# Performance work log

Hardware: AMD Instinct MI355X
Metric: run time of the kernel (lower is better)

Reference implementation:

```python
import jax, jax.numpy as jnp
import numpy as np

B, N, D, C = 1, 512, 128, 128
EPS = 1e-5


def _layernorm(x, g, b):
    m = jnp.mean(x, axis=-1, keepdims=True)
    v = jnp.mean(jnp.square(x - m), axis=-1, keepdims=True)
    return (x - m) * jax.lax.rsqrt(v + EPS) * g + b


def setup_inputs() -> dict:
    key = jax.random.key(0)
    ks = jax.random.split(key, 14)
    sD = 1.0 / np.sqrt(D)
    sC = 1.0 / np.sqrt(C)

    def w(k, shape, scale):
        return jax.random.normal(k, shape, dtype=jnp.float32) * scale

    return {
        "x": jax.random.normal(ks[0], (B, N, N, D), dtype=jnp.float32),
        "ln_in_g": jnp.ones((D,), jnp.float32),
        "ln_in_b": jnp.zeros((D,), jnp.float32),
        "ln_out_g": jnp.ones((C,), jnp.float32),
        "ln_out_b": jnp.zeros((C,), jnp.float32),
        "Wl": w(ks[1], (D, C), sD), "bl": w(ks[2], (C,), 0.02),
        "Wr": w(ks[3], (D, C), sD), "br": w(ks[4], (C,), 0.02),
        "Wo": w(ks[5], (C, D), sC), "bo": w(ks[6], (D,), 0.02),
        "Wlg": w(ks[7], (D, C), sD), "blg": w(ks[8], (C,), 0.02),
        "Wrg": w(ks[9], (D, C), sD), "brg": w(ks[10], (C,), 0.02),
        "Wog": w(ks[11], (D, D), sD), "bog": w(ks[12], (D,), 0.02),
    }


def reference(x, ln_in_g, ln_in_b, ln_out_g, ln_out_b,
              Wl, bl, Wr, br, Wo, bo, Wlg, blg, Wrg, brg, Wog, bog):
    # x: [B, N, N, D] pair representation
    xn = _layernorm(x, ln_in_g, ln_in_b)
    left = jax.nn.sigmoid(xn @ Wlg + blg) * (xn @ Wl + bl)    # [B,N,N,C]
    right = jax.nn.sigmoid(xn @ Wrg + brg) * (xn @ Wr + br)   # [B,N,N,C]
    # type='out': contract over k (rows): out[b,i,j,c] = sum_k left[b,k,i,c]*right[b,k,j,c]
    out = jnp.einsum('bkic,bkjc->bijc', left, right)           # [B,N,N,C]
    out = jax.nn.sigmoid(xn @ Wog + bog) * (_layernorm(out, ln_out_g, ln_out_b) @ Wo + bo)
    return out
```

## Files before the change

kernel.cpp:

```cpp
#include <hip/hip_runtime.h>
#include <hip/hip_bf16.h>
#include <cstdint>
#include <cstddef>

typedef unsigned short u16;
typedef short bf16x8 __attribute__((ext_vector_type(8)));
typedef float f32x4 __attribute__((ext_vector_type(4)));

constexpr int Ns = 512;
constexpr int Dd = 128;
constexpr int Cc = 128;
#define EPSV 1e-5f

__device__ __forceinline__ u16 f2bf(float f){
    __hip_bfloat16 h = __float2bfloat16(f);
    return *reinterpret_cast<u16*>(&h);
}
__device__ __forceinline__ float bf2f(u16 h){
    return __uint_as_float(((uint32_t)h) << 16);
}
__device__ __forceinline__ float sigmoidf_(float x){
    return 1.0f / (1.0f + __expf(-x));
}

__global__ void k_prep(const float* __restrict__ Wl, const float* __restrict__ Wlg,
                       const float* __restrict__ Wr, const float* __restrict__ Wrg,
                       const float* __restrict__ Wog, const float* __restrict__ Wo,
                       u16* __restrict__ Wt){
    int idx = blockIdx.x * 256 + threadIdx.x;
    if (idx >= 6 * 16384) return;
    int m = idx >> 14; int nk = idx & 16383; int n = nk >> 7; int k = nk & 127;
    const float* W = (m == 0) ? Wl : (m == 1) ? Wlg : (m == 2) ? Wr
                   : (m == 3) ? Wrg : (m == 4) ? Wog : Wo;
    Wt[idx] = f2bf(W[k * Cc + n]);
}

__global__ __launch_bounds__(256) void k1(
    const float* __restrict__ x, const float* __restrict__ g_ln, const float* __restrict__ b_ln,
    const u16* __restrict__ Wt,
    const float* __restrict__ bl, const float* __restrict__ blg,
    const float* __restrict__ br, const float* __restrict__ brg,
    const float* __restrict__ bog,
    u16* __restrict__ left, u16* __restrict__ right, u16* __restrict__ og)
{
    __shared__ u16  lA[64][136];
    __shared__ u16  lS[64][132];
    __shared__ float gln[128], bln[128];

    const int t   = threadIdx.x;
    const int bid = blockIdx.x;
    const int a0  = (bid >> 6) << 3;
    const int b0  = (bid & 63) << 3;
    const int w = t >> 6, l = t & 63;
    const int lrow = l & 15, g = l >> 4;
    const int nb = w * 32;
    const int orow = g << 2;
    const int kb = a0 >> 3;

    auto LOADP = [&](int mV, int mG, int cf, bf16x8 (&bv)[4], bf16x8 (&bg)[4]){
        const u16* WV = Wt + (size_t)mV * 16384;
        const u16* WG = Wt + (size_t)mG * 16384;
        const int col = nb + cf * 16 + lrow;
#pragma unroll
        for (int ks = 0; ks < 4; ++ks){
            bv[ks] = *reinterpret_cast<const bf16x8*>(WV + (size_t)col * 128 + ks * 32 + g * 8);
            bg[ks] = *reinterpret_cast<const bf16x8*>(WG + (size_t)col * 128 + ks * 32 + g * 8);
        }
    };
    auto LOAD1 = [&](int mV, int cf, bf16x8 (&bv)[4]){
        const u16* WV = Wt + (size_t)mV * 16384;
        const int col = nb + cf * 16 + lrow;
#pragma unroll
        for (int ks = 0; ks < 4; ++ks)
            bv[ks] = *reinterpret_cast<const bf16x8*>(WV + (size_t)col * 128 + ks * 32 + g * 8);
    };

    const int r = t >> 2, q = t & 3;
    const int aa = a0 + (r & 7), bb = b0 + (r >> 3);
    const float4* xrow = reinterpret_cast<const float4*>(x + ((size_t)aa * Ns + bb) * Dd);
    float4 xv[8];
#pragma unroll
    for (int i2 = 0; i2 < 8; ++i2) xv[i2] = xrow[q + 4 * i2];

    bf16x8 bvA[4], bgA[4], bvB[4], bgB[4];
    LOADP(0, 1, 0, bvA, bgA);

    if (t < 128){ gln[t] = g_ln[t]; bln[t] = b_ln[t]; }

    float s1 = 0.f, s2 = 0.f;
#pragma unroll
    for (int i2 = 0; i2 < 8; ++i2){
        float4 v = xv[i2];
        s1 += v.x + v.y + v.z + v.w;
        s2 += v.x * v.x + v.y * v.y + v.z * v.z + v.w * v.w;
    }
    s1 += __shfl_xor(s1, 1); s1 += __shfl_xor(s1, 2);
    s2 += __shfl_xor(s2, 1); s2 += __shfl_xor(s2, 2);
    const float mm  = s1 * (1.0f / 128.0f);
    const float rsv = rsqrtf(s2 * (1.0f / 128.0f) - mm * mm + EPSV);
    __syncthreads();
#pragma unroll
    for (int i2 = 0; i2 < 8; ++i2){
        const int d = (q + 4 * i2) * 4;
        ushort4 o;
        o.x = f2bf((xv[i2].x - mm) * rsv * gln[d + 0] + bln[d + 0]);
        o.y = f2bf((xv[i2].y - mm) * rsv * gln[d + 1] + bln[d + 1]);
        o.z = f2bf((xv[i2].z - mm) * rsv * gln[d + 2] + bln[d + 2]);
        o.w = f2bf((xv[i2].w - mm) * rsv * gln[d + 3] + bln[d + 3]);
        *reinterpret_cast<ushort4*>(&lA[r][d]) = o;
    }
    __syncthreads();

    bf16x8 af[4][4];
#pragma unroll
    for (int ks = 0; ks < 4; ++ks)
#pragma unroll
        for (int rf = 0; rf < 4; ++rf)
            af[ks][rf] = *reinterpret_cast<const bf16x8*>(&lA[rf * 16 + lrow][ks * 32 + g * 8]);

    const f32x4 zero4 = {0.f, 0.f, 0.f, 0.f};
    f32x4 aV[4], aG[4];
    auto Z2 = [&](){
#pragma unroll
        for (int rf = 0; rf < 4; ++rf){ aV[rf] = zero4; aG[rf] = zero4; }
    };
    auto MMVG = [&](const bf16x8 (&bv)[4], const bf16x8 (&bg)[4]){
#pragma unroll
        for (int ks = 0; ks < 4; ++ks){
#pragma unroll
            for (int rf = 0; rf < 4; ++rf)
                aV[rf] = __builtin_amdgcn_mfma_f32_16x16x32_bf16(af[ks][rf], bv[ks], aV[rf], 0, 0, 0);
#pragma unroll
            for (int rf = 0; rf < 4; ++rf)
                aG[rf] = __builtin_amdgcn_mfma_f32_16x16x32_bf16(af[ks][rf], bg[ks], aG[rf], 0, 0, 0);
        }
    };
    auto MMV = [&](const bf16x8 (&bv)[4]){
#pragma unroll
        for (int ks = 0; ks < 4; ++ks)
#pragma unroll
            for (int rf = 0; rf < 4; ++rf)
                aV[rf] = __builtin_amdgcn_mfma_f32_16x16x32_bf16(af[ks][rf], bv[ks], aV[rf], 0, 0, 0);
    };
    auto EPI1 = [&](u16* dst, const float* bV, const float* bG, int cf){
        const int col = nb + cf * 16 + lrow;
        const float bVv = bV[col], bGv = bG[col];
#pragma unroll
        for (int rf = 0; rf < 4; ++rf){
            ushort4 pk;
#pragma unroll
            for (int j = 0; j < 4; ++j){
                const float vv = aV[rf][j] + bVv;
                const float gg = aG[rf][j] + bGv;
                ((u16*)&pk)[j] = f2bf(sigmoidf_(gg) * vv);
            }
            const size_t base = (((size_t)col * 64 + kb) * Ns + b0 + rf * 2 + (orow >> 3)) * 8 + (orow & 4);
            *reinterpret_cast<ushort4*>(dst + base) = pk;
        }
    };
    auto OG1 = [&](int cf){
        const int col = nb + cf * 16 + lrow;
        const float bOv = bog[col];
#pragma unroll
        for (int rf = 0; rf < 4; ++rf)
#pragma unroll
            for (int j = 0; j < 4; ++j){
                const int row = rf * 16 + orow + j;
                lS[row][col] = f2bf(sigmoidf_(aV[rf][j] + bOv));
            }
    };

    LOADP(0, 1, 1, bvB, bgB);
    Z2(); MMVG(bvA, bgA); EPI1(left, bl, blg, 0);
    LOADP(2, 3, 0, bvA, bgA);
    Z2(); MMVG(bvB, bgB); EPI1(left, bl, blg, 1);
    LOADP(2, 3, 1, bvB, bgB);
    Z2(); MMVG(bvA, bgA); EPI1(right, br, brg, 0);
    LOAD1(4, 0, bvA);
    Z2(); MMVG(bvB, bgB); EPI1(right, br, brg, 1);
    LOAD1(4, 1, bvB);
#pragma unroll
    for (int rf = 0; rf < 4; ++rf) aV[rf] = zero4;
    MMV(bvA); OG1(0);
#pragma unroll
    for (int rf = 0; rf < 4; ++rf) aV[rf] = zero4;
    MMV(bvB); OG1(1);

    __syncthreads();
    const int bsub = t >> 5, c4 = (t & 31) * 4;
#pragma unroll
    for (int a = 0; a < 8; ++a){
        const int row = bsub * 8 + a;
        int2 v = *reinterpret_cast<const int2*>(&lS[row][c4]);
        *reinterpret_cast<int2*>(og + (((size_t)(a0 + a) * Ns) + (b0 + bsub)) * Cc + c4) = v;
    }
}

#define K2_LOAD(AF, BF, KS) do {                                                    \
    const size_t kbrow_ = (size_t)((KS) * 4 + lkb) * Ns;                            \
    _Pragma("unroll") for (int rf = 0; rf < 4; ++rf)                                \
        AF[rf] = *reinterpret_cast<const bf16x8*>(Lc + (kbrow_ + ib + rf * 16 + lrow) * 8); \
    _Pragma("unroll") for (int cf = 0; cf < 4; ++cf)                                \
        BF[cf] = *reinterpret_cast<const bf16x8*>(Rc + (kbrow_ + jb + cf * 16 + lrow) * 8); \
} while (0)

#define K2_MM(AF, BF) do {                                                          \
    _Pragma("unroll") for (int rf = 0; rf < 4; ++rf)                                \
    _Pragma("unroll") for (int cf = 0; cf < 4; ++cf)                                \
        acc[rf][cf] = __builtin_amdgcn_mfma_f32_16x16x32_bf16(AF[rf], BF[cf], acc[rf][cf], 0, 0, 0); \
} while (0)

__global__ __launch_bounds__(256) void k2(const u16* __restrict__ left,
                                          const u16* __restrict__ right,
                                          u16* __restrict__ om)
{
    __shared__ u16 sO[128][136];
    const int bid = blockIdx.x;
    const int xcd = bid & 7, idxx = bid >> 3;
    const int virt = xcd * 256 + idxx;
    const int c    = virt >> 4;
    const int tile = virt & 15;
    const int iy = tile >> 2, jx = tile & 3;
    const int t = threadIdx.x, w = t >> 6, l = t & 63;
    const int wr = w >> 1, wc = w & 1;
    const int ib = iy * 128 + wr * 64;
    const int jb = jx * 128 + wc * 64;
    const int lrow = l & 15, lkb = l >> 4;
    const u16* Lc = left  + (size_t)c * (Ns * Ns);
    const u16* Rc = right + (size_t)c * (Ns * Ns);
    const f32x4 zero4 = {0.f, 0.f, 0.f, 0.f};
    f32x4 acc[4][4];
#pragma unroll
    for (int rf = 0; rf < 4; ++rf)
#pragma unroll
        for (int cf = 0; cf < 4; ++cf) acc[rf][cf] = zero4;

    bf16x8 a0f[4], b0f[4], a1f[4], b1f[4];
    K2_LOAD(a0f, b0f, 0);
#pragma unroll
    for (int ks = 0; ks < 16; ks += 2){
        K2_LOAD(a1f, b1f, ks + 1);
        K2_MM(a0f, b0f);
        if (ks + 2 < 16) K2_LOAD(a0f, b0f, ks + 2);
        K2_MM(a1f, b1f);
    }

    const int orow = (l >> 4) << 2;
#pragma unroll
    for (int rf = 0; rf < 4; ++rf)
#pragma unroll
        for (int j2 = 0; j2 < 4; ++j2){
            const int rloc = wr * 64 + rf * 16 + orow + j2;
#pragma unroll
            for (int cf = 0; cf < 4; ++cf)
                sO[rloc][wc * 64 + cf * 16 + lrow] = f2bf(acc[rf][cf][j2]);
        }
    __syncthreads();
    u16* obase = om + (size_t)c * Ns * Ns + (size_t)(iy * 128) * Ns + jx * 128;
#pragma unroll
    for (int s = 0; s < 8; ++s){
        const int gg = s * 256 + t;
        const int row = gg >> 4, co = (gg & 15) * 8;
        int4 v = *reinterpret_cast<const int4*>(&sO[row][co]);
        *reinterpret_cast<int4*>(obase + (size_t)row * Ns + co) = v;
    }
}

__global__ __launch_bounds__(256) void k3(
    const u16* __restrict__ om, const u16* __restrict__ og, const u16* __restrict__ Wt,
    const float* __restrict__ g2, const float* __restrict__ b2, const float* __restrict__ bo,
    float* __restrict__ out)
{
    __shared__ char smem[34816];
    u16* X = reinterpret_cast<u16*>(smem);
    u16* O = reinterpret_cast<u16*>(smem) + 8704;
    __shared__ float sg2[128], sb2[128];
    const int i  = blockIdx.y;
    const int j0 = blockIdx.x * 64;
    const int t  = threadIdx.x;
    if (t < 128){ sg2[t] = g2[t]; sb2[t] = b2[t]; }
    {
        const int c = t >> 1, jh = (t & 1) * 32;
        const u16* src = om + (size_t)c * Ns * Ns + (size_t)i * Ns + j0 + jh;
#pragma unroll
        for (int s = 0; s < 8; ++s){
            ushort4 v = reinterpret_cast<const ushort4*>(src)[s];
            const int jj = jh + s * 4;
            X[(jj + 0) * 136 + c] = v.x; X[(jj + 1) * 136 + c] = v.y;
            X[(jj + 2) * 136 + c] = v.z; X[(jj + 3) * 136 + c] = v.w;
        }
    }
    {
        const int jj = t >> 2, qq = t & 3;
        const u16* src = og + ((size_t)i * Ns + j0 + jj) * Cc + qq * 32;
#pragma unroll
        for (int s = 0; s < 4; ++s)
            *reinterpret_cast<int4*>(&O[jj * 136 + qq * 32 + s * 8]) = reinterpret_cast<const int4*>(src)[s];
    }
    __syncthreads();
    const int r = t >> 2, q = t & 3;
    {
        float s1 = 0.f, s2v = 0.f;
#pragma unroll
        for (int e = 0; e < 32; ++e){
            const float v = bf2f(X[r * 136 + q * 32 + e]);
            s1 += v; s2v += v * v;
        }
        s1  += __shfl_xor(s1, 1);  s1  += __shfl_xor(s1, 2);
        s2v += __shfl_xor(s2v, 1); s2v += __shfl_xor(s2v, 2);
        const float mm  = s1 * (1.0f / 128.0f);
        const float rsv = rsqrtf(s2v * (1.0f / 128.0f) - mm * mm + EPSV);
#pragma unroll
        for (int e = 0; e < 32; ++e){
            const int cc = q * 32 + e;
            const float v = bf2f(X[r * 136 + cc]);
            X[r * 136 + cc] = f2bf((v - mm) * rsv * sg2[cc] + sb2[cc]);
        }
    }
    __syncthreads();
    const int w = t >> 6, l = t & 63;
    const int lrow = l & 15, lk = (l >> 4) << 3, nbv = w * 32, orow = (l >> 4) << 2;
    const u16* WO = Wt + (size_t)5 * 16384;
    const f32x4 zero4 = {0.f, 0.f, 0.f, 0.f};
    f32x4 acc[4][2];
#pragma unroll
    for (int rf = 0; rf < 4; ++rf)
#pragma unroll
        for (int cf = 0; cf < 2; ++cf) acc[rf][cf] = zero4;
#pragma unroll
    for (int ks = 0; ks < 4; ++ks){
        const int k0 = ks * 32 + lk;
        bf16x8 af[4];
#pragma unroll
        for (int rf = 0; rf < 4; ++rf)
            af[rf] = *reinterpret_cast<const bf16x8*>(&X[(rf * 16 + lrow) * 136 + k0]);
#pragma unroll
        for (int cf = 0; cf < 2; ++cf){
            bf16x8 bv = *reinterpret_cast<const bf16x8*>(WO + (size_t)(nbv + cf * 16 + lrow) * 128 + k0);
#pragma unroll
            for (int rf = 0; rf < 4; ++rf)
                acc[rf][cf] = __builtin_amdgcn_mfma_f32_16x16x32_bf16(af[rf], bv, acc[rf][cf], 0, 0, 0);
        }
    }
    float gv[2][4][4];
#pragma unroll
    for (int cf = 0; cf < 2; ++cf){
        const int cg = nbv + cf * 16 + lrow;
        const float bov = bo[cg];
#pragma unroll
        for (int rf = 0; rf < 4; ++rf)
#pragma unroll
            for (int j = 0; j < 4; ++j){
                const int row = rf * 16 + orow + j;
                gv[cf][rf][j] = bf2f(O[row * 136 + cg]) * (acc[rf][cf][j] + bov);
            }
    }
    __syncthreads();
    float* sF = reinterpret_cast<float*>(smem);
#pragma unroll
    for (int cf = 0; cf < 2; ++cf){
        const int cg = nbv + cf * 16 + lrow;
#pragma unroll
        for (int rf = 0; rf < 4; ++rf)
#pragma unroll
            for (int j = 0; j < 4; ++j){
                const int row = rf * 16 + orow + j;
                sF[row * 128 + cg] = gv[cf][rf][j];
            }
    }
    __syncthreads();
    const float4* sF4 = reinterpret_cast<const float4*>(smem);
    float* obase = out + ((size_t)i * Ns + j0) * Cc;
#pragma unroll
    for (int s = 0; s < 8; ++s){
        const int gg = s * 256 + t;
        const int row = gg >> 5, co = (gg & 31) * 4;
        float4 v = sF4[gg];
        *reinterpret_cast<float4*>(obase + (size_t)row * Cc + co) = v;
    }
}

extern "C" void kernel_launch(void* const* d_in, const int* in_sizes, int n_in,
                              void* d_out, int out_size, void* d_ws, size_t ws_size,
                              hipStream_t stream)
{
    const float* x    = (const float*)d_in[0];
    const float* ling = (const float*)d_in[1];
    const float* linb = (const float*)d_in[2];
    const float* loutg= (const float*)d_in[3];
    const float* loutb= (const float*)d_in[4];
    const float* Wl   = (const float*)d_in[5];
    const float* bl   = (const float*)d_in[6];
    const float* Wr   = (const float*)d_in[7];
    const float* br   = (const float*)d_in[8];
    const float* Wo   = (const float*)d_in[9];
    const float* bo   = (const float*)d_in[10];
    const float* Wlg  = (const float*)d_in[11];
    const float* blg  = (const float*)d_in[12];
    const float* Wrg  = (const float*)d_in[13];
    const float* brg  = (const float*)d_in[14];
    const float* Wog  = (const float*)d_in[15];
    const float* bog  = (const float*)d_in[16];

    char* ws = (char*)d_ws;
    u16* Wt = (u16*)ws;
    const size_t off = 256 * 1024;
    const size_t SZ  = (size_t)33554432 * 2;
    u16* left  = (u16*)(ws + off);
    u16* right = (u16*)(ws + off + SZ);
    u16* og    = (u16*)(ws + off + 2 * SZ);
    u16* om    = (u16*)(ws + off + 3 * SZ);

    hipLaunchKernelGGL(k_prep, dim3(384), dim3(256), 0, stream, Wl, Wlg, Wr, Wrg, Wog, Wo, Wt);
    hipLaunchKernelGGL(k1, dim3(4096), dim3(256), 0, stream,
                       x, ling, linb, Wt, bl, blg, br, brg, bog, left, right, og);
    hipLaunchKernelGGL(k2, dim3(2048), dim3(256), 0, stream, left, right, om);
    hipLaunchKernelGGL(k3, dim3(8, 512), dim3(256), 0, stream, om, og, Wt, loutg, loutb, bo, (float*)d_out);
}
```

Measured before the change: 270.0 us.

## Stage left/right outputs through shared memory for coalesced stores, drop weight prefetch

The k1 kernel now writes the gated left/right projections into a single reused shared buffer and then stores them to global memory as 16-byte rows. Previously each lane issued scattered 8-byte stores. The explicit double-buffered weight register prefetch is replaced by loads inline with the MFMA loop, which lowers register pressure but exposes load latency. Sigmoid now uses the hardware reciprocal, and the og GEMM loop is kept rolled. Extra __syncthreads barriers are added between phases.

Measured after the change: 254.1 us, median of 2. 1.06x faster.

```diff
diff --git a/kernel.cpp b/kernel.cpp
--- a/kernel.cpp
+++ b/kernel.cpp
@@ -20,7 +20,7 @@
     return __uint_as_float(((uint32_t)h) << 16);
 }
 __device__ __forceinline__ float sigmoidf_(float x){
-    return 1.0f / (1.0f + __expf(-x));
+    return __builtin_amdgcn_rcpf(1.0f + __expf(-x));
 }
 
 __global__ void k_prep(const float* __restrict__ Wl, const float* __restrict__ Wlg,
@@ -43,8 +43,7 @@
     const float* __restrict__ bog,
     u16* __restrict__ left, u16* __restrict__ right, u16* __restrict__ og)
 {
-    __shared__ u16  lA[64][136];
-    __shared__ u16  lS[64][132];
+    __shared__ u16  SB[8704];
     __shared__ float gln[128], bln[128];
 
     const int t   = threadIdx.x;
@@ -57,34 +56,12 @@
     const int orow = g << 2;
     const int kb = a0 >> 3;
 
-    auto LOADP = [&](int mV, int mG, int cf, bf16x8 (&bv)[4], bf16x8 (&bg)[4]){
-        const u16* WV = Wt + (size_t)mV * 16384;
-        const u16* WG = Wt + (size_t)mG * 16384;
-        const int col = nb + cf * 16 + lrow;
-#pragma unroll
-        for (int ks = 0; ks < 4; ++ks){
-            bv[ks] = *reinterpret_cast<const bf16x8*>(WV + (size_t)col * 128 + ks * 32 + g * 8);
-            bg[ks] = *reinterpret_cast<const bf16x8*>(WG + (size_t)col * 128 + ks * 32 + g * 8);
-        }
-    };
-    auto LOAD1 = [&](int mV, int cf, bf16x8 (&bv)[4]){
-        const u16* WV = Wt + (size_t)mV * 16384;
-        const int col = nb + cf * 16 + lrow;
-#pragma unroll
-        for (int ks = 0; ks < 4; ++ks)
-            bv[ks] = *reinterpret_cast<const bf16x8*>(WV + (size_t)col * 128 + ks * 32 + g * 8);
-    };
-
     const int r = t >> 2, q = t & 3;
     const int aa = a0 + (r & 7), bb = b0 + (r >> 3);
     const float4* xrow = reinterpret_cast<const float4*>(x + ((size_t)aa * Ns + bb) * Dd);
     float4 xv[8];
 #pragma unroll
     for (int i2 = 0; i2 < 8; ++i2) xv[i2] = xrow[q + 4 * i2];
-
-    bf16x8 bvA[4], bgA[4], bvB[4], bgB[4];
-    LOADP(0, 1, 0, bvA, bgA);
-
     if (t < 128){ gln[t] = g_ln[t]; bln[t] = b_ln[t]; }
 
     float s1 = 0.f, s2 = 0.f;
@@ -107,7 +84,7 @@
         o.y = f2bf((xv[i2].y - mm) * rsv * gln[d + 1] + bln[d + 1]);
         o.z = f2bf((xv[i2].z - mm) * rsv * gln[d + 2] + bln[d + 2]);
         o.w = f2bf((xv[i2].w - mm) * rsv * gln[d + 3] + bln[d + 3]);
-        *reinterpret_cast<ushort4*>(&lA[r][d]) = o;
+        *reinterpret_cast<ushort4*>(&SB[r * 136 + d]) = o;
     }
     __syncthreads();
 
@@ -116,33 +93,29 @@
     for (int ks = 0; ks < 4; ++ks)
 #pragma unroll
         for (int rf = 0; rf < 4; ++rf)
-            af[ks][rf] = *reinterpret_cast<const bf16x8*>(&lA[rf * 16 + lrow][ks * 32 + g * 8]);
+            af[ks][rf] = *reinterpret_cast<const bf16x8*>(&SB[(rf * 16 + lrow) * 136 + ks * 32 + g * 8]);
+    __syncthreads();
 
     const f32x4 zero4 = {0.f, 0.f, 0.f, 0.f};
     f32x4 aV[4], aG[4];
-    auto Z2 = [&](){
+
+    auto GEMM1 = [&](const u16* WV, const u16* WG, int cf){
+        const int col = nb + cf * 16 + lrow;
 #pragma unroll
         for (int rf = 0; rf < 4; ++rf){ aV[rf] = zero4; aG[rf] = zero4; }
+#pragma unroll
+        for (int ks = 0; ks < 4; ++ks){
+            bf16x8 bv = *reinterpret_cast<const bf16x8*>(WV + (size_t)col * 128 + ks * 32 + g * 8);
+            bf16x8 bg = *reinterpret_cast<const bf16x8*>(WG + (size_t)col * 128 + ks * 32 + g * 8);
+#pragma unroll
+            for (int rf = 0; rf < 4; ++rf)
+                aV[rf] = __builtin_amdgcn_mfma_f32_16x16x32_bf16(af[ks][rf], bv, aV[rf], 0, 0, 0);
+#pragma unroll
+            for (int rf = 0; rf < 4; ++rf)
+                aG[rf] = __builtin_amdgcn_mfma_f32_16x16x32_bf16(af[ks][rf], bg, aG[rf], 0, 0, 0);
+        }
     };
-    auto MMVG = [&](const bf16x8 (&bv)[4], const bf16x8 (&bg)[4]){
-#pragma unroll
-        for (int ks = 0; ks < 4; ++ks){
-#pragma unroll
-            for (int rf = 0; rf < 4; ++rf)
-                aV[rf] = __builtin_amdgcn_mfma_f32_16x16x32_bf16(af[ks][rf], bv[ks], aV[rf], 0, 0, 0);
-#pragma unroll
-            for (int rf = 0; rf < 4; ++rf)
-                aG[rf] = __builtin_amdgcn_mfma_f32_16x16x32_bf16(af[ks][rf], bg[ks], aG[rf], 0, 0, 0);
-        }
-    };
-    auto MMV = [&](const bf16x8 (&bv)[4]){
-#pragma unroll
-        for (int ks = 0; ks < 4; ++ks)
-#pragma unroll
-            for (int rf = 0; rf < 4; ++rf)
-                aV[rf] = __builtin_amdgcn_mfma_f32_16x16x32_bf16(af[ks][rf], bv[ks], aV[rf], 0, 0, 0);
-    };
-    auto EPI1 = [&](u16* dst, const float* bV, const float* bG, int cf){
+    auto STW = [&](const float* bV, const float* bG, int cf){
         const int col = nb + cf * 16 + lrow;
         const float bVv = bV[col], bGv = bG[col];
 #pragma unroll
@@ -154,44 +127,58 @@
                 const float gg = aG[rf][j] + bGv;
                 ((u16*)&pk)[j] = f2bf(sigmoidf_(gg) * vv);
             }
-            const size_t base = (((size_t)col * 64 + kb) * Ns + b0 + rf * 2 + (orow >> 3)) * 8 + (orow & 4);
-            *reinterpret_cast<ushort4*>(dst + base) = pk;
+            *reinterpret_cast<ushort4*>(&SB[col * 68 + rf * 16 + orow]) = pk;
         }
     };
-    auto OG1 = [&](int cf){
+    auto STORE = [&](u16* dst){
+#pragma unroll
+        for (int it = 0; it < 4; ++it){
+            const int cl = it * 32 + (t >> 3);
+            const int s  = t & 7;
+            int4 v = *reinterpret_cast<const int4*>(&SB[cl * 68 + s * 8]);
+            *reinterpret_cast<int4*>(dst + (((size_t)cl * 64 + kb) * Ns + b0) * 8 + s * 8) = v;
+        }
+    };
+
+    GEMM1(Wt,             Wt + 16384,     0); STW(bl, blg, 0);
+    GEMM1(Wt,             Wt + 16384,     1); STW(bl, blg, 1);
+    __syncthreads();
+    STORE(left);
+    __syncthreads();
+    GEMM1(Wt + 2 * 16384, Wt + 3 * 16384, 0); STW(br, brg, 0);
+    GEMM1(Wt + 2 * 16384, Wt + 3 * 16384, 1); STW(br, brg, 1);
+    __syncthreads();
+    STORE(right);
+    __syncthreads();
+
+    const u16* WO = Wt + (size_t)4 * 16384;
+#pragma unroll 1
+    for (int cf = 0; cf < 2; ++cf){
         const int col = nb + cf * 16 + lrow;
+#pragma unroll
+        for (int rf = 0; rf < 4; ++rf) aV[rf] = zero4;
+#pragma unroll
+        for (int ks = 0; ks < 4; ++ks){
+            bf16x8 bv = *reinterpret_cast<const bf16x8*>(WO + (size_t)col * 128 + ks * 32 + g * 8);
+#pragma unroll
+            for (int rf = 0; rf < 4; ++rf)
+                aV[rf] = __builtin_amdgcn_mfma_f32_16x16x32_bf16(af[ks][rf], bv, aV[rf], 0, 0, 0);
+        }
         const float bOv = bog[col];
 #pragma unroll
         for (int rf = 0; rf < 4; ++rf)
 #pragma unroll
             for (int j = 0; j < 4; ++j){
                 const int row = rf * 16 + orow + j;
-                lS[row][col] = f2bf(sigmoidf_(aV[rf][j] + bOv));
+                SB[row * 132 + col] = f2bf(sigmoidf_(aV[rf][j] + bOv));
             }
-    };
-
-    LOADP(0, 1, 1, bvB, bgB);
-    Z2(); MMVG(bvA, bgA); EPI1(left, bl, blg, 0);
-    LOADP(2, 3, 0, bvA, bgA);
-    Z2(); MMVG(bvB, bgB); EPI1(left, bl, blg, 1);
-    LOADP(2, 3, 1, bvB, bgB);
-    Z2(); MMVG(bvA, bgA); EPI1(right, br, brg, 0);
-    LOAD1(4, 0, bvA);
-    Z2(); MMVG(bvB, bgB); EPI1(right, br, brg, 1);
-    LOAD1(4, 1, bvB);
-#pragma unroll
-    for (int rf = 0; rf < 4; ++rf) aV[rf] = zero4;
-    MMV(bvA); OG1(0);
-#pragma unroll
-    for (int rf = 0; rf < 4; ++rf) aV[rf] = zero4;
-    MMV(bvB); OG1(1);
-
+    }
     __syncthreads();
     const int bsub = t >> 5, c4 = (t & 31) * 4;
 #pragma unroll
     for (int a = 0; a < 8; ++a){
         const int row = bsub * 8 + a;
-        int2 v = *reinterpret_cast<const int2*>(&lS[row][c4]);
+        int2 v = *reinterpret_cast<const int2*>(&SB[row * 132 + c4]);
         *reinterpret_cast<int2*>(og + (((size_t)(a0 + a) * Ns) + (b0 + bsub)) * Cc + c4) = v;
     }
 }
```
